# Kernel optimization log

Measured on AMD Instinct MI355X. Metric: run time of the kernel, lower is better.

The kernel has to match this reference:

```python
import jax, jax.numpy as jnp
import numpy as np

NUM_CODES = 8192
EMBED_DIM = 256
N_TOKENS = 65536
COMMITMENT_COST = 0.25


def setup_inputs() -> dict:
    key = jax.random.key(0)
    k1, k2 = jax.random.split(key)
    inputs = jax.random.normal(k1, (N_TOKENS, EMBED_DIM), dtype=jnp.float32)
    # torch init: uniform(-1/num_codes, 1/num_codes); use normal-scale equivalent via uniform
    weight = jax.random.uniform(k2, (NUM_CODES, EMBED_DIM), dtype=jnp.float32,
                                minval=-1.0 / NUM_CODES, maxval=1.0 / NUM_CODES)
    return {"inputs": inputs, "weight": weight}


def reference(inputs, weight):
    inputs_sq = jnp.sum(inputs * inputs, axis=1, keepdims=True)      # (N, 1)
    embed_sq = jnp.sum(weight * weight, axis=1)                      # (K,)
    distances = inputs_sq + embed_sq - 2.0 * (inputs @ weight.T)     # (N, K)
    indices = jnp.argmin(distances, axis=1)                          # (N,)
    quantized = jnp.take(weight, indices, axis=0)                    # (N, D)

    codebook_loss = jnp.mean((quantized - jax.lax.stop_gradient(inputs)) ** 2)
    commit_loss = jnp.mean((inputs - jax.lax.stop_gradient(quantized)) ** 2)
    vq_loss = codebook_loss + COMMITMENT_COST * commit_loss

    # straight-through estimator
    quantized_st = inputs + jax.lax.stop_gradient(quantized - inputs)
    return quantized_st, indices, vq_loss, codebook_loss, commit_loss
```

## Files before the change

kernel.cpp:

```cpp
#include <hip/hip_runtime.h>

#define N_TOK  65536
#define N_CODE 8192
#define DIM    256

typedef _Float16 f16;
typedef _Float16 f16x8 __attribute__((ext_vector_type(8)));
typedef float    f32x4 __attribute__((ext_vector_type(4)));

__global__ __launch_bounds__(256) void rowsq_kernel(const float* __restrict__ src,
                                                    float* __restrict__ dst, int nrows) {
    int row  = blockIdx.x * 4 + (threadIdx.x >> 6);
    int lane = threadIdx.x & 63;
    if (row >= nrows) return;
    float4 v = ((const float4*)(src + (size_t)row * DIM))[lane];
    float s = v.x * v.x + v.y * v.y + v.z * v.z + v.w * v.w;
#pragma unroll
    for (int off = 32; off; off >>= 1) s += __shfl_down(s, off, 64);
    if (lane == 0) dst[row] = s;
}

__global__ __launch_bounds__(256) void splitw_t_kernel(const float* __restrict__ W,
                                                       f16* __restrict__ W1t,
                                                       f16* __restrict__ W2t) {
    int g = blockIdx.x * 256 + threadIdx.x;
    int o = g >> 13;
    int c = g & 8191;
    const float* p = W + (size_t)c * DIM + o * 8;
    float4 v0 = ((const float4*)p)[0];
    float4 v1 = ((const float4*)p)[1];
    float e[8] = {v0.x, v0.y, v0.z, v0.w, v1.x, v1.y, v1.z, v1.w};
    union { f16 h[8]; uint4 u; } p1, p2;
#pragma unroll
    for (int i = 0; i < 8; ++i) {
        float ws = e[i] * 16384.0f;
        f16 w1 = (f16)ws;
        float r = (ws - (float)w1) * 2048.0f;
        p1.h[i] = w1; p2.h[i] = (f16)r;
    }
    size_t byteoff = (size_t)o * 131072 + (size_t)c * 16;
    *(uint4*)((char*)W1t + byteoff) = p1.u;
    *(uint4*)((char*)W2t + byteoff) = p2.u;
}

__global__ __launch_bounds__(256, 2) void argmin_mfma8(
    const float* __restrict__ X, const f16* __restrict__ W1t, const f16* __restrict__ W2t,
    const float* __restrict__ sxq, const float* __restrict__ esq,
    int* __restrict__ out_idx) {

    __shared__ char wbuf[65536];

    const int tid  = threadIdx.x;
    const int lane = tid & 63;
    const int wv   = tid >> 6;
    const int cl   = lane & 15;
    const int q    = lane >> 4;
    const int l5   = lane >> 5;
    const int lane31 = lane & 31;
    const int wavetok0 = blockIdx.x * 128 + wv * 32;

    f16x8 a1[2][8], a2[2][8];
#pragma unroll
    for (int mt = 0; mt < 2; ++mt)
#pragma unroll
        for (int s = 0; s < 8; ++s) {
            const float* p = X + (size_t)(wavetok0 + mt * 16 + cl) * DIM + s * 32 + q * 8;
            float4 v0 = ((const float4*)p)[0];
            float4 v1 = ((const float4*)p)[1];
            float e[8] = {v0.x, v0.y, v0.z, v0.w, v1.x, v1.y, v1.z, v1.w};
#pragma unroll
            for (int j = 0; j < 8; ++j) {
                f16 h = (f16)e[j];
                float r = (e[j] - (float)h) * 2048.0f;
                a1[mt][s][j] = h;
                a2[mt][s][j] = (f16)r;
            }
        }

    float sxr[8];
#pragma unroll
    for (int mt = 0; mt < 2; ++mt)
#pragma unroll
        for (int r = 0; r < 4; ++r)
            sxr[mt * 4 + r] = sxq[wavetok0 + mt * 16 + q * 4 + r];

    float bestd[8];
    int   besti[8];
#pragma unroll
    for (int i = 0; i < 8; ++i) { bestd[i] = 3.4e38f; besti[i] = 0x7fffffff; }

    const int SL = l5 * 131072 + lane31 * 16;
    const char* RB = wbuf + q * 512 + cl * 16;

    auto stage = [&](int ct2, int sel) {
        const char* g1 = (const char*)W1t + ct2 * 512 + SL;
        const char* g2 = (const char*)W2t + ct2 * 512 + SL;
#pragma unroll
        for (int t = 0; t < 8; ++t) {
            int fi = wv * 8 + t;
            int L  = fi >> 4;
            int op = fi & 15;
            const char* gsrc = (L ? g2 : g1) + op * 262144;
            char* ldst = wbuf + sel * 32768 + L * 16384 + op * 1024;
            __builtin_amdgcn_global_load_lds(
                (const __attribute__((address_space(1))) unsigned int*)gsrc,
                (__attribute__((address_space(3))) unsigned int*)ldst, 16, 0, 0);
        }
    };

    stage(0, 0);
    __syncthreads();

    for (int ct = 0; ct < N_CODE / 32; ++ct) {
        if (ct + 1 < N_CODE / 32) stage(ct + 1, (ct + 1) & 1);

        float se0 = esq[ct * 32 + cl];
        float se1 = esq[ct * 32 + 16 + cl];

        f32x4 mainA[2][2], cross[2][2];
#pragma unroll
        for (int mt = 0; mt < 2; ++mt)
#pragma unroll
            for (int nt = 0; nt < 2; ++nt) {
                mainA[mt][nt] = (f32x4){0.f, 0.f, 0.f, 0.f};
                cross[mt][nt] = (f32x4){0.f, 0.f, 0.f, 0.f};
            }

        const char* va = RB + ((ct & 1) << 15);
#pragma unroll
        for (int s = 0; s < 8; ++s) {
            f16x8 b1[2], b2[2];
            b1[0] = *(const f16x8*)(va + s * 2048);
            b1[1] = *(const f16x8*)(va + s * 2048 + 256);
            b2[0] = *(const f16x8*)(va + s * 2048 + 16384);
            b2[1] = *(const f16x8*)(va + s * 2048 + 16640);
            __builtin_amdgcn_s_setprio(1);
#pragma unroll
            for (int mt = 0; mt < 2; ++mt)
#pragma unroll
                for (int nt = 0; nt < 2; ++nt) {
                    mainA[mt][nt] = __builtin_amdgcn_mfma_f32_16x16x32_f16(a1[mt][s], b1[nt], mainA[mt][nt], 0, 0, 0);
                    cross[mt][nt] = __builtin_amdgcn_mfma_f32_16x16x32_f16(a2[mt][s], b1[nt], cross[mt][nt], 0, 0, 0);
                    cross[mt][nt] = __builtin_amdgcn_mfma_f32_16x16x32_f16(a1[mt][s], b2[nt], cross[mt][nt], 0, 0, 0);
                }
            __builtin_amdgcn_s_setprio(0);
        }

#pragma unroll
        for (int mt = 0; mt < 2; ++mt)
#pragma unroll
            for (int nt = 0; nt < 2; ++nt)
#pragma unroll
                for (int r = 0; r < 4; ++r) {
                    float mc = fmaf(cross[mt][nt][r], 4.8828125e-4f, mainA[mt][nt][r]);
                    float t1 = sxr[mt * 4 + r] + (nt ? se1 : se0);
                    float d  = fmaf(-1.220703125e-4f, mc, t1);
                    int slot = mt * 4 + r;
                    if (d < bestd[slot]) {
                        bestd[slot] = d;
                        besti[slot] = ct * 32 + nt * 16 + cl;
                    }
                }
        __syncthreads();
    }

#pragma unroll
    for (int slot = 0; slot < 8; ++slot) {
        float d = bestd[slot];
        int   i = besti[slot];
#pragma unroll
        for (int off = 1; off < 16; off <<= 1) {
            float od = __shfl_xor(d, off, 64);
            int   oi = __shfl_xor(i, off, 64);
            if (od < d || (od == d && oi < i)) { d = od; i = oi; }
        }
        if (cl == 0)
            out_idx[wavetok0 + (slot >> 2) * 16 + q * 4 + (slot & 3)] = i;
    }
}

__global__ __launch_bounds__(256) void finalize_kernel(
    const float* __restrict__ X, const float* __restrict__ W,
    const int* __restrict__ idx, float* __restrict__ outQ,
    float* __restrict__ outI, double* __restrict__ accum) {
    __shared__ double wsum[4];
    int wid  = threadIdx.x >> 6;
    int lane = threadIdx.x & 63;
    int token = blockIdx.x * 4 + wid;
    int id = idx[token];
    float4 x = ((const float4*)(X + (size_t)token * DIM))[lane];
    float4 qv = ((const float4*)(W + (size_t)id * DIM))[lane];
    float4 o;
    o.x = x.x + (qv.x - x.x);
    o.y = x.y + (qv.y - x.y);
    o.z = x.z + (qv.z - x.z);
    o.w = x.w + (qv.w - x.w);
    ((float4*)(outQ + (size_t)token * DIM))[lane] = o;
    float dx = x.x - qv.x, dy = x.y - qv.y, dz = x.z - qv.z, dw = x.w - qv.w;
    float s = dx * dx + dy * dy + dz * dz + dw * dw;
#pragma unroll
    for (int off = 32; off; off >>= 1) s += __shfl_down(s, off, 64);
    if (lane == 0) {
        outI[token] = (float)id;
        wsum[wid] = (double)s;
    }
    __syncthreads();
    if (threadIdx.x == 0) {
        double t = wsum[0] + wsum[1] + wsum[2] + wsum[3];
        atomicAdd(&accum[blockIdx.x & 127], t);
    }
}

__global__ void scalars_kernel(const double* __restrict__ accum, float* __restrict__ out) {
    double mse = 0.0;
    for (int i = 0; i < 128; ++i) mse += accum[i];
    mse /= (double)((size_t)N_TOK * DIM);
    float c = (float)mse;
    out[0] = c + 0.25f * c;
    out[1] = c;
    out[2] = c;
}

extern "C" void kernel_launch(void* const* d_in, const int* in_sizes, int n_in,
                              void* d_out, int out_size, void* d_ws, size_t ws_size,
                              hipStream_t stream) {
    const float* X = (const float*)d_in[0];
    const float* W = (const float*)d_in[1];

    float* outQ = (float*)d_out;
    float* outI = outQ + (size_t)N_TOK * DIM;
    float* outS = outI + N_TOK;

    char* ws = (char*)d_ws;
    double* accum = (double*)ws;
    float* esq = (float*)(ws + 4096);
    float* sxq = (float*)(ws + 4096 + 32768);
    int*   idx = (int*)(ws + 4096 + 32768 + 262144);
    f16*   W1t = (f16*)(ws + (1 << 20));
    f16*   W2t = (f16*)(ws + (1 << 20) + 4194304);

    hipMemsetAsync(accum, 0, 128 * sizeof(double), stream);
    splitw_t_kernel<<<N_CODE * 32 / 256, 256, 0, stream>>>(W, W1t, W2t);
    rowsq_kernel<<<N_CODE / 4, 256, 0, stream>>>(W, esq, N_CODE);
    rowsq_kernel<<<N_TOK / 4, 256, 0, stream>>>(X, sxq, N_TOK);
    argmin_mfma8<<<N_TOK / 128, 256, 0, stream>>>(X, W1t, W2t, sxq, esq, idx);
    finalize_kernel<<<N_TOK / 4, 256, 0, stream>>>(X, W, idx, outQ, outI, accum);
    scalars_kernel<<<1, 1, 0, stream>>>(accum, outS);
}
```

Baseline: 745.1 us.

## Shrink argmin tiles to 64 tokens x 16 codes with 2-wave blocks

Restructures the argmin MFMA kernel to use 128-thread blocks covering 64 tokens, stepping 16 codes per iteration instead of 32, with half the LDS staging buffer. This cuts accumulator registers and LDS per block so more blocks fit per CU and there are twice as many blocks. In exchange, each staged codebook tile is reused by fewer tokens, so global/LDS traffic per FLOP doubles, and there are twice as many loop iterations and barriers.

```diff
diff --git a/kernel.cpp b/kernel.cpp
--- a/kernel.cpp
+++ b/kernel.cpp
@@ -43,21 +43,19 @@
     *(uint4*)((char*)W2t + byteoff) = p2.u;
 }
 
-__global__ __launch_bounds__(256, 2) void argmin_mfma8(
+__global__ __launch_bounds__(128, 2) void argmin_mfma9(
     const float* __restrict__ X, const f16* __restrict__ W1t, const f16* __restrict__ W2t,
     const float* __restrict__ sxq, const float* __restrict__ esq,
     int* __restrict__ out_idx) {
 
-    __shared__ char wbuf[65536];
+    __shared__ char wbuf[32768];
 
     const int tid  = threadIdx.x;
     const int lane = tid & 63;
     const int wv   = tid >> 6;
     const int cl   = lane & 15;
     const int q    = lane >> 4;
-    const int l5   = lane >> 5;
-    const int lane31 = lane & 31;
-    const int wavetok0 = blockIdx.x * 128 + wv * 32;
+    const int wavetok0 = blockIdx.x * 64 + wv * 32;
 
     f16x8 a1[2][8], a2[2][8];
 #pragma unroll
@@ -89,19 +87,19 @@
 #pragma unroll
     for (int i = 0; i < 8; ++i) { bestd[i] = 3.4e38f; besti[i] = 0x7fffffff; }
 
-    const int SL = l5 * 131072 + lane31 * 16;
-    const char* RB = wbuf + q * 512 + cl * 16;
+    const int SLB = (lane >> 4) * 131072 + (lane & 15) * 16;
+    const char* RB = wbuf + q * 256 + cl * 16;
 
     auto stage = [&](int ct2, int sel) {
-        const char* g1 = (const char*)W1t + ct2 * 512 + SL;
-        const char* g2 = (const char*)W2t + ct2 * 512 + SL;
+        const char* g1 = (const char*)W1t + ct2 * 256 + SLB;
+        const char* g2 = (const char*)W2t + ct2 * 256 + SLB;
 #pragma unroll
         for (int t = 0; t < 8; ++t) {
             int fi = wv * 8 + t;
-            int L  = fi >> 4;
-            int op = fi & 15;
-            const char* gsrc = (L ? g2 : g1) + op * 262144;
-            char* ldst = wbuf + sel * 32768 + L * 16384 + op * 1024;
+            int L  = fi >> 3;
+            int op = fi & 7;
+            const char* gsrc = (L ? g2 : g1) + op * 524288;
+            char* ldst = wbuf + sel * 16384 + L * 8192 + op * 1024;
             __builtin_amdgcn_global_load_lds(
                 (const __attribute__((address_space(1))) unsigned int*)gsrc,
                 (__attribute__((address_space(3))) unsigned int*)ldst, 16, 0, 0);
@@ -111,56 +109,46 @@
     stage(0, 0);
     __syncthreads();
 
-    for (int ct = 0; ct < N_CODE / 32; ++ct) {
-        if (ct + 1 < N_CODE / 32) stage(ct + 1, (ct + 1) & 1);
-
-        float se0 = esq[ct * 32 + cl];
-        float se1 = esq[ct * 32 + 16 + cl];
-
-        f32x4 mainA[2][2], cross[2][2];
+    for (int ct = 0; ct < N_CODE / 16; ++ct) {
+        if (ct + 1 < N_CODE / 16) stage(ct + 1, (ct + 1) & 1);
+
+        float se = esq[ct * 16 + cl];
+
+        f32x4 mainA[2], cross[2];
+#pragma unroll
+        for (int mt = 0; mt < 2; ++mt) {
+            mainA[mt] = (f32x4){0.f, 0.f, 0.f, 0.f};
+            cross[mt] = (f32x4){0.f, 0.f, 0.f, 0.f};
+        }
+
+        const char* va = RB + ((ct & 1) << 14);
+#pragma unroll
+        for (int s = 0; s < 8; ++s) {
+            f16x8 b1 = *(const f16x8*)(va + s * 1024);
+            f16x8 b2 = *(const f16x8*)(va + s * 1024 + 8192);
+            __builtin_amdgcn_s_setprio(1);
+#pragma unroll
+            for (int mt = 0; mt < 2; ++mt) {
+                mainA[mt] = __builtin_amdgcn_mfma_f32_16x16x32_f16(a1[mt][s], b1, mainA[mt], 0, 0, 0);
+                cross[mt] = __builtin_amdgcn_mfma_f32_16x16x32_f16(a2[mt][s], b1, cross[mt], 0, 0, 0);
+                cross[mt] = __builtin_amdgcn_mfma_f32_16x16x32_f16(a1[mt][s], b2, cross[mt], 0, 0, 0);
+            }
+            __builtin_amdgcn_s_setprio(0);
+        }
+
 #pragma unroll
         for (int mt = 0; mt < 2; ++mt)
 #pragma unroll
-            for (int nt = 0; nt < 2; ++nt) {
-                mainA[mt][nt] = (f32x4){0.f, 0.f, 0.f, 0.f};
-                cross[mt][nt] = (f32x4){0.f, 0.f, 0.f, 0.f};
+            for (int r = 0; r < 4; ++r) {
+                float mc = fmaf(cross[mt][r], 4.8828125e-4f, mainA[mt][r]);
+                float t1 = sxr[mt * 4 + r] + se;
+                float d  = fmaf(-1.220703125e-4f, mc, t1);
+                int slot = mt * 4 + r;
+                if (d < bestd[slot]) {
+                    bestd[slot] = d;
+                    besti[slot] = ct * 16 + cl;
+                }
             }
-
-        const char* va = RB + ((ct & 1) << 15);
-#pragma unroll
-        for (int s = 0; s < 8; ++s) {
-            f16x8 b1[2], b2[2];
-            b1[0] = *(const f16x8*)(va + s * 2048);
-            b1[1] = *(const f16x8*)(va + s * 2048 + 256);
-            b2[0] = *(const f16x8*)(va + s * 2048 + 16384);
-            b2[1] = *(const f16x8*)(va + s * 2048 + 16640);
-            __builtin_amdgcn_s_setprio(1);
-#pragma unroll
-            for (int mt = 0; mt < 2; ++mt)
-#pragma unroll
-                for (int nt = 0; nt < 2; ++nt) {
-                    mainA[mt][nt] = __builtin_amdgcn_mfma_f32_16x16x32_f16(a1[mt][s], b1[nt], mainA[mt][nt], 0, 0, 0);
-                    cross[mt][nt] = __builtin_amdgcn_mfma_f32_16x16x32_f16(a2[mt][s], b1[nt], cross[mt][nt], 0, 0, 0);
-                    cross[mt][nt] = __builtin_amdgcn_mfma_f32_16x16x32_f16(a1[mt][s], b2[nt], cross[mt][nt], 0, 0, 0);
-                }
-            __builtin_amdgcn_s_setprio(0);
-        }
-
-#pragma unroll
-        for (int mt = 0; mt < 2; ++mt)
-#pragma unroll
-            for (int nt = 0; nt < 2; ++nt)
-#pragma unroll
-                for (int r = 0; r < 4; ++r) {
-                    float mc = fmaf(cross[mt][nt][r], 4.8828125e-4f, mainA[mt][nt][r]);
-                    float t1 = sxr[mt * 4 + r] + (nt ? se1 : se0);
-                    float d  = fmaf(-1.220703125e-4f, mc, t1);
-                    int slot = mt * 4 + r;
-                    if (d < bestd[slot]) {
-                        bestd[slot] = d;
-                        besti[slot] = ct * 32 + nt * 16 + cl;
-                    }
-                }
         __syncthreads();
     }
 
@@ -243,7 +231,7 @@
     splitw_t_kernel<<<N_CODE * 32 / 256, 256, 0, stream>>>(W, W1t, W2t);
     rowsq_kernel<<<N_CODE / 4, 256, 0, stream>>>(W, esq, N_CODE);
     rowsq_kernel<<<N_TOK / 4, 256, 0, stream>>>(X, sxq, N_TOK);
-    argmin_mfma8<<<N_TOK / 128, 256, 0, stream>>>(X, W1t, W2t, sxq, esq, idx);
+    argmin_mfma9<<<N_TOK / 64, 128, 0, stream>>>(X, W1t, W2t, sxq, esq, idx);
     finalize_kernel<<<N_TOK / 4, 256, 0, stream>>>(X, W, idx, outQ, outI, accum);
     scalars_kernel<<<1, 1, 0, stream>>>(accum, outS);
 }
```

New measurement: 838.9 us. 1.13x slower.

## Software-pipeline argmin epilogue with next tile's MFMAs using ping-pong accumulators

Applied to the files above, without the earlier changes.

Adds a second set of accumulators so that the distance/argmin epilogue for tile ct-1 is issued after the MFMAs for tile ct. This lets VALU compare work overlap with matrix-core execution instead of stalling on MFMA results. The s_setprio hints around the MFMA block are removed. Costs: 32 more accumulator VGPRs, which may spill or reduce occupancy under launch_bounds(256,2).

```diff
diff --git a/kernel.cpp b/kernel.cpp
--- a/kernel.cpp
+++ b/kernel.cpp
@@ -43,7 +43,7 @@
     *(uint4*)((char*)W2t + byteoff) = p2.u;
 }
 
-__global__ __launch_bounds__(256, 2) void argmin_mfma8(
+__global__ __launch_bounds__(256, 2) void argmin_mfma10(
     const float* __restrict__ X, const f16* __restrict__ W1t, const f16* __restrict__ W2t,
     const float* __restrict__ sxq, const float* __restrict__ esq,
     int* __restrict__ out_idx) {
@@ -89,12 +89,12 @@
 #pragma unroll
     for (int i = 0; i < 8; ++i) { bestd[i] = 3.4e38f; besti[i] = 0x7fffffff; }
 
-    const int SL = l5 * 131072 + lane31 * 16;
+    const int SLB = l5 * 131072 + lane31 * 16;
     const char* RB = wbuf + q * 512 + cl * 16;
 
     auto stage = [&](int ct2, int sel) {
-        const char* g1 = (const char*)W1t + ct2 * 512 + SL;
-        const char* g2 = (const char*)W2t + ct2 * 512 + SL;
+        const char* g1 = (const char*)W1t + ct2 * 512 + SLB;
+        const char* g2 = (const char*)W2t + ct2 * 512 + SLB;
 #pragma unroll
         for (int t = 0; t < 8; ++t) {
             int fi = wv * 8 + t;
@@ -108,24 +108,41 @@
         }
     };
 
-    stage(0, 0);
-    __syncthreads();
-
-    for (int ct = 0; ct < N_CODE / 32; ++ct) {
+    f32x4 Am[2][2], Ac[2][2], Bm[2][2], Bc[2][2];
+    float se0A = 0.f, se1A = 0.f, se0B = 0.f, se1B = 0.f;
+
+    auto epi = [&](f32x4 (&pm)[2][2], f32x4 (&pc)[2][2], float s0, float s1, int ctp) {
+#pragma unroll
+        for (int mt = 0; mt < 2; ++mt)
+#pragma unroll
+            for (int nt = 0; nt < 2; ++nt)
+#pragma unroll
+                for (int r = 0; r < 4; ++r) {
+                    float mc = fmaf(pc[mt][nt][r], 4.8828125e-4f, pm[mt][nt][r]);
+                    float t1 = sxr[mt * 4 + r] + (nt ? s1 : s0);
+                    float d  = fmaf(-1.220703125e-4f, mc, t1);
+                    int slot = mt * 4 + r;
+                    if (d < bestd[slot]) {
+                        bestd[slot] = d;
+                        besti[slot] = ctp * 32 + nt * 16 + cl;
+                    }
+                }
+    };
+
+    auto tile_step = [&](int ct, f32x4 (&cm)[2][2], f32x4 (&cc)[2][2],
+                         float& c0, float& c1,
+                         f32x4 (&pm)[2][2], f32x4 (&pc)[2][2],
+                         float p0, float p1, bool doEpi) {
         if (ct + 1 < N_CODE / 32) stage(ct + 1, (ct + 1) & 1);
-
-        float se0 = esq[ct * 32 + cl];
-        float se1 = esq[ct * 32 + 16 + cl];
-
-        f32x4 mainA[2][2], cross[2][2];
+        c0 = esq[ct * 32 + cl];
+        c1 = esq[ct * 32 + 16 + cl];
 #pragma unroll
         for (int mt = 0; mt < 2; ++mt)
 #pragma unroll
             for (int nt = 0; nt < 2; ++nt) {
-                mainA[mt][nt] = (f32x4){0.f, 0.f, 0.f, 0.f};
-                cross[mt][nt] = (f32x4){0.f, 0.f, 0.f, 0.f};
+                cm[mt][nt] = (f32x4){0.f, 0.f, 0.f, 0.f};
+                cc[mt][nt] = (f32x4){0.f, 0.f, 0.f, 0.f};
             }
-
         const char* va = RB + ((ct & 1) << 15);
 #pragma unroll
         for (int s = 0; s < 8; ++s) {
@@ -134,35 +151,29 @@
             b1[1] = *(const f16x8*)(va + s * 2048 + 256);
             b2[0] = *(const f16x8*)(va + s * 2048 + 16384);
             b2[1] = *(const f16x8*)(va + s * 2048 + 16640);
-            __builtin_amdgcn_s_setprio(1);
 #pragma unroll
             for (int mt = 0; mt < 2; ++mt)
 #pragma unroll
                 for (int nt = 0; nt < 2; ++nt) {
-                    mainA[mt][nt] = __builtin_amdgcn_mfma_f32_16x16x32_f16(a1[mt][s], b1[nt], mainA[mt][nt], 0, 0, 0);
-                    cross[mt][nt] = __builtin_amdgcn_mfma_f32_16x16x32_f16(a2[mt][s], b1[nt], cross[mt][nt], 0, 0, 0);
-                    cross[mt][nt] = __builtin_amdgcn_mfma_f32_16x16x32_f16(a1[mt][s], b2[nt], cross[mt][nt], 0, 0, 0);
+                    cm[mt][nt] = __builtin_amdgcn_mfma_f32_16x16x32_f16(a1[mt][s], b1[nt], cm[mt][nt], 0, 0, 0);
+                    cc[mt][nt] = __builtin_amdgcn_mfma_f32_16x16x32_f16(a2[mt][s], b1[nt], cc[mt][nt], 0, 0, 0);
+                    cc[mt][nt] = __builtin_amdgcn_mfma_f32_16x16x32_f16(a1[mt][s], b2[nt], cc[mt][nt], 0, 0, 0);
                 }
-            __builtin_amdgcn_s_setprio(0);
-        }
-
-#pragma unroll
-        for (int mt = 0; mt < 2; ++mt)
-#pragma unroll
-            for (int nt = 0; nt < 2; ++nt)
-#pragma unroll
-                for (int r = 0; r < 4; ++r) {
-                    float mc = fmaf(cross[mt][nt][r], 4.8828125e-4f, mainA[mt][nt][r]);
-                    float t1 = sxr[mt * 4 + r] + (nt ? se1 : se0);
-                    float d  = fmaf(-1.220703125e-4f, mc, t1);
-                    int slot = mt * 4 + r;
-                    if (d < bestd[slot]) {
-                        bestd[slot] = d;
-                        besti[slot] = ct * 32 + nt * 16 + cl;
-                    }
-                }
+        }
+        if (doEpi) epi(pm, pc, p0, p1, ct - 1);
         __syncthreads();
-    }
+    };
+
+    stage(0, 0);
+    __syncthreads();
+
+    tile_step(0, Am, Ac, se0A, se1A, Bm, Bc, se0B, se1B, false);
+    for (int k = 1; k < 254; k += 2) {
+        tile_step(k,     Bm, Bc, se0B, se1B, Am, Ac, se0A, se1A, true);
+        tile_step(k + 1, Am, Ac, se0A, se1A, Bm, Bc, se0B, se1B, true);
+    }
+    tile_step(255, Bm, Bc, se0B, se1B, Am, Ac, se0A, se1A, true);
+    epi(Bm, Bc, se0B, se1B, 255);
 
 #pragma unroll
     for (int slot = 0; slot < 8; ++slot) {
@@ -243,7 +254,7 @@
     splitw_t_kernel<<<N_CODE * 32 / 256, 256, 0, stream>>>(W, W1t, W2t);
     rowsq_kernel<<<N_CODE / 4, 256, 0, stream>>>(W, esq, N_CODE);
     rowsq_kernel<<<N_TOK / 4, 256, 0, stream>>>(X, sxq, N_TOK);
-    argmin_mfma8<<<N_TOK / 128, 256, 0, stream>>>(X, W1t, W2t, sxq, esq, idx);
+    argmin_mfma10<<<N_TOK / 128, 256, 0, stream>>>(X, W1t, W2t, sxq, esq, idx);
     finalize_kernel<<<N_TOK / 4, 256, 0, stream>>>(X, W, idx, outQ, outI, accum);
     scalars_kernel<<<1, 1, 0, stream>>>(accum, outS);
 }
```

New measurement: 1.597 ms. +114.4%, slower.

## Software-pipeline argmin epilogue across code tiles with ping-pong accumulators

Applied to the files above, without the earlier changes.

Uses two sets of accumulator registers so that the distance/argmin epilogue for the previous 32-code tile is interleaved, two entries per k-step, with the MFMA chain of the current tile. The goal is to hide the scalar compare/select work behind matrix-core execution rather than running it serially after each tile's MFMAs. It doubles the accumulator register footprint, which may pressure the 2-waves-per-SIMD occupancy target, and it adds a manually peeled final epilogue.

```diff
diff --git a/kernel.cpp b/kernel.cpp
--- a/kernel.cpp
+++ b/kernel.cpp
@@ -43,7 +43,7 @@
     *(uint4*)((char*)W2t + byteoff) = p2.u;
 }
 
-__global__ __launch_bounds__(256, 2) void argmin_mfma8(
+__global__ __launch_bounds__(256, 2) void argmin_mfma11(
     const float* __restrict__ X, const f16* __restrict__ W1t, const f16* __restrict__ W2t,
     const float* __restrict__ sxq, const float* __restrict__ esq,
     int* __restrict__ out_idx) {
@@ -89,12 +89,12 @@
 #pragma unroll
     for (int i = 0; i < 8; ++i) { bestd[i] = 3.4e38f; besti[i] = 0x7fffffff; }
 
-    const int SL = l5 * 131072 + lane31 * 16;
+    const int SLB = l5 * 131072 + lane31 * 16;
     const char* RB = wbuf + q * 512 + cl * 16;
 
     auto stage = [&](int ct2, int sel) {
-        const char* g1 = (const char*)W1t + ct2 * 512 + SL;
-        const char* g2 = (const char*)W2t + ct2 * 512 + SL;
+        const char* g1 = (const char*)W1t + ct2 * 512 + SLB;
+        const char* g2 = (const char*)W2t + ct2 * 512 + SLB;
 #pragma unroll
         for (int t = 0; t < 8; ++t) {
             int fi = wv * 8 + t;
@@ -108,60 +108,77 @@
         }
     };
 
+    const f32x4 Z = (f32x4){0.f, 0.f, 0.f, 0.f};
+
+#define VQ_TILE(CT, cm, cc, c0, c1, pm, pc, p0, p1, DOEPI)                          \
+    {                                                                                \
+        if ((CT) + 1 < N_CODE / 32) stage((CT) + 1, ((CT) + 1) & 1);                 \
+        c0 = esq[(CT) * 32 + cl];                                                    \
+        c1 = esq[(CT) * 32 + 16 + cl];                                               \
+        const char* va = RB + (((CT) & 1) << 15);                                    \
+        _Pragma("unroll")                                                            \
+        for (int s = 0; s < 8; ++s) {                                                \
+            f16x8 b1f[2], b2f[2];                                                    \
+            b1f[0] = *(const f16x8*)(va + s * 2048);                                 \
+            b1f[1] = *(const f16x8*)(va + s * 2048 + 256);                           \
+            b2f[0] = *(const f16x8*)(va + s * 2048 + 16384);                         \
+            b2f[1] = *(const f16x8*)(va + s * 2048 + 16640);                         \
+            __builtin_amdgcn_s_setprio(1);                                           \
+            _Pragma("unroll")                                                        \
+            for (int m2 = 0; m2 < 2; ++m2)                                           \
+                _Pragma("unroll")                                                    \
+                for (int n2 = 0; n2 < 2; ++n2) {                                     \
+                    cm[m2][n2] = __builtin_amdgcn_mfma_f32_16x16x32_f16(             \
+                        a1[m2][s], b1f[n2], s ? cm[m2][n2] : Z, 0, 0, 0);            \
+                    cc[m2][n2] = __builtin_amdgcn_mfma_f32_16x16x32_f16(             \
+                        a2[m2][s], b1f[n2], s ? cc[m2][n2] : Z, 0, 0, 0);            \
+                    cc[m2][n2] = __builtin_amdgcn_mfma_f32_16x16x32_f16(             \
+                        a1[m2][s], b2f[n2], cc[m2][n2], 0, 0, 0);                    \
+                }                                                                    \
+            __builtin_amdgcn_s_setprio(0);                                           \
+            if (DOEPI) {                                                             \
+                _Pragma("unroll")                                                    \
+                for (int e = 2 * s; e < 2 * s + 2; ++e) {                            \
+                    const int emt = e >> 3, ent = (e >> 2) & 1, er = e & 3;          \
+                    float mc = fmaf(pc[emt][ent][er], 4.8828125e-4f,                 \
+                                    pm[emt][ent][er]);                               \
+                    float t1 = sxr[emt * 4 + er] + (ent ? p1 : p0);                  \
+                    float d  = fmaf(-1.220703125e-4f, mc, t1);                       \
+                    const int slot = emt * 4 + er;                                   \
+                    if (d < bestd[slot]) {                                           \
+                        bestd[slot] = d;                                             \
+                        besti[slot] = ((CT) - 1) * 32 + ent * 16 + cl;               \
+                    }                                                                \
+                }                                                                    \
+            }                                                                        \
+        }                                                                            \
+        __syncthreads();                                                             \
+    }
+
     stage(0, 0);
     __syncthreads();
 
-    for (int ct = 0; ct < N_CODE / 32; ++ct) {
-        if (ct + 1 < N_CODE / 32) stage(ct + 1, (ct + 1) & 1);
-
-        float se0 = esq[ct * 32 + cl];
-        float se1 = esq[ct * 32 + 16 + cl];
-
-        f32x4 mainA[2][2], cross[2][2];
-#pragma unroll
-        for (int mt = 0; mt < 2; ++mt)
-#pragma unroll
-            for (int nt = 0; nt < 2; ++nt) {
-                mainA[mt][nt] = (f32x4){0.f, 0.f, 0.f, 0.f};
-                cross[mt][nt] = (f32x4){0.f, 0.f, 0.f, 0.f};
-            }
-
-        const char* va = RB + ((ct & 1) << 15);
-#pragma unroll
-        for (int s = 0; s < 8; ++s) {
-            f16x8 b1[2], b2[2];
-            b1[0] = *(const f16x8*)(va + s * 2048);
-            b1[1] = *(const f16x8*)(va + s * 2048 + 256);
-            b2[0] = *(const f16x8*)(va + s * 2048 + 16384);
-            b2[1] = *(const f16x8*)(va + s * 2048 + 16640);
-            __builtin_amdgcn_s_setprio(1);
-#pragma unroll
-            for (int mt = 0; mt < 2; ++mt)
-#pragma unroll
-                for (int nt = 0; nt < 2; ++nt) {
-                    mainA[mt][nt] = __builtin_amdgcn_mfma_f32_16x16x32_f16(a1[mt][s], b1[nt], mainA[mt][nt], 0, 0, 0);
-                    cross[mt][nt] = __builtin_amdgcn_mfma_f32_16x16x32_f16(a2[mt][s], b1[nt], cross[mt][nt], 0, 0, 0);
-                    cross[mt][nt] = __builtin_amdgcn_mfma_f32_16x16x32_f16(a1[mt][s], b2[nt], cross[mt][nt], 0, 0, 0);
-                }
-            __builtin_amdgcn_s_setprio(0);
-        }
-
-#pragma unroll
-        for (int mt = 0; mt < 2; ++mt)
-#pragma unroll
-            for (int nt = 0; nt < 2; ++nt)
-#pragma unroll
-                for (int r = 0; r < 4; ++r) {
-                    float mc = fmaf(cross[mt][nt][r], 4.8828125e-4f, mainA[mt][nt][r]);
-                    float t1 = sxr[mt * 4 + r] + (nt ? se1 : se0);
-                    float d  = fmaf(-1.220703125e-4f, mc, t1);
-                    int slot = mt * 4 + r;
-                    if (d < bestd[slot]) {
-                        bestd[slot] = d;
-                        besti[slot] = ct * 32 + nt * 16 + cl;
-                    }
-                }
-        __syncthreads();
+    f32x4 Am[2][2], Ac[2][2], Bm[2][2], Bc[2][2];
+    float seA0 = 0.f, seA1 = 0.f, seB0 = 0.f, seB1 = 0.f;
+
+    VQ_TILE(0, Am, Ac, seA0, seA1, Bm, Bc, seB0, seB1, false)
+    for (int k = 1; k < 254; k += 2) {
+        VQ_TILE(k,     Bm, Bc, seB0, seB1, Am, Ac, seA0, seA1, true)
+        VQ_TILE(k + 1, Am, Ac, seA0, seA1, Bm, Bc, seB0, seB1, true)
+    }
+    VQ_TILE(255, Bm, Bc, seB0, seB1, Am, Ac, seA0, seA1, true)
+
+#pragma unroll
+    for (int e = 0; e < 16; ++e) {
+        const int emt = e >> 3, ent = (e >> 2) & 1, er = e & 3;
+        float mc = fmaf(Bc[emt][ent][er], 4.8828125e-4f, Bm[emt][ent][er]);
+        float t1 = sxr[emt * 4 + er] + (ent ? seB1 : seB0);
+        float d  = fmaf(-1.220703125e-4f, mc, t1);
+        const int slot = emt * 4 + er;
+        if (d < bestd[slot]) {
+            bestd[slot] = d;
+            besti[slot] = 255 * 32 + ent * 16 + cl;
+        }
     }
 
 #pragma unroll
@@ -243,7 +260,7 @@
     splitw_t_kernel<<<N_CODE * 32 / 256, 256, 0, stream>>>(W, W1t, W2t);
     rowsq_kernel<<<N_CODE / 4, 256, 0, stream>>>(W, esq, N_CODE);
     rowsq_kernel<<<N_TOK / 4, 256, 0, stream>>>(X, sxq, N_TOK);
-    argmin_mfma8<<<N_TOK / 128, 256, 0, stream>>>(X, W1t, W2t, sxq, esq, idx);
+    argmin_mfma11<<<N_TOK / 128, 256, 0, stream>>>(X, W1t, W2t, sxq, esq, idx);
     finalize_kernel<<<N_TOK / 4, 256, 0, stream>>>(X, W, idx, outQ, outI, accum);
     scalars_kernel<<<1, 1, 0, stream>>>(accum, outS);
 }
```

After: 767.8 us. 1.03x slower.
